# Performance work log

Hardware: AMD Instinct MI355X
Metric: run time of the kernel (lower is better)

Reference implementation:

```python
import jax, jax.numpy as jnp
import numpy as np

B_GR = 128    # graphs per batch
N0 = 512      # nodes per graph before pooling
E_PER = 4096  # edges per graph (kept static; pooled-away edges get weight 0)
H = 128       # hidden
F = 128       # num_features (== hidden)
C = 10        # num_classes
K_HOP = 3     # Jacobi polynomial order (hop_num)
A_J, B_J = 1.0, 1.0
EPS = 1e-5


def _bn(h, g, b):
    # training-mode BatchNorm1d: batch stats, biased variance
    m = jnp.mean(h, 0)
    v = jnp.mean((h - m) ** 2, 0)
    return (h - m) * jax.lax.rsqrt(v + EPS) * g + b


def _forward(x, convW, convb, bnW, bnB, bn7W, bn7B, attW, theta,
             lin1W, lin1b, lin2W, lin2b, lin3W, lin3b, src, dst):
    w = jnp.ones((src.shape[0],), x.dtype)  # edge weights; 0 => filtered edge
    n = N0
    h = x
    reads = []
    for i in range(5):
        N = B_GR * n
        # symmetric GCN normalization with self loops on the weighted graph
        deg = jax.ops.segment_sum(w, dst, num_segments=N) + 1.0
        dinv = jax.lax.rsqrt(deg)
        enorm = dinv[src] * dinv[dst] * w   # per-edge norm [E]
        snorm = dinv * dinv                 # self-loop norm [N]
        prop = lambda m_: jax.ops.segment_sum(enorm[:, None] * m_[src], dst, num_segments=N) + m_ * snorm[:, None]
        pvec = lambda v_: jax.ops.segment_sum(enorm * v_[src], dst, num_segments=N) + v_ * snorm
        # GCNConv -> BN -> ReLU
        h = prop(h @ convW[i]) + convb[i]
        h = jax.nn.relu(_bn(h, bnW[i], bnB[i]))
        # JacobiPool: Jacobi-polynomial diffusion of attention scores
        s0 = h @ attW[i]                    # [N]
        polys = [s0, 0.5 * ((A_J - B_J) * s0 + (A_J + B_J + 2.0) * pvec(s0))]
        for kk in range(2, K_HOP + 1):
            c0 = 2 * kk * (kk + A_J + B_J) * (2 * kk + A_J + B_J - 2)
            c1 = (2 * kk + A_J + B_J - 1) * (2 * kk + A_J + B_J) * (2 * kk + A_J + B_J - 2)
            c2 = (2 * kk + A_J + B_J - 1) * (A_J * A_J - B_J * B_J)
            c3 = 2 * (kk + A_J - 1) * (kk + B_J - 1) * (2 * kk + A_J + B_J)
            polys.append((c1 * pvec(polys[-1]) + c2 * polys[-1] - c3 * polys[-2]) / c0)
        score = sum(theta[i, j] * polys[j] for j in range(K_HOP + 1))
        # top-k node selection per graph (ratio 0.5 -> static k)
        k = n // 2
        _, idx = jax.lax.top_k(score.reshape(B_GR, n), k)
        sel = (idx + (jnp.arange(B_GR) * n)[:, None]).reshape(-1)  # global node ids [B*k]
        h = h[sel] * jnp.tanh(score[sel])[:, None]
        # remap/filter edges to surviving nodes (masked, static edge count)
        new_id = jnp.full((N,), -1, jnp.int32).at[sel].set(jnp.arange(B_GR * k, dtype=jnp.int32))
        ns, nd = new_id[src], new_id[dst]
        valid = (ns >= 0) & (nd >= 0) & (w > 0)
        w = valid.astype(x.dtype)
        src = jnp.where(valid, ns, 0)
        dst = jnp.where(valid, nd, 0)
        # readout: global max pool || global mean pool per graph
        xg = h.reshape(B_GR, k, H)
        reads.append(jnp.concatenate([xg.max(1), xg.mean(1)], -1))
        n = k
    g = sum(reads) / 5.0                    # [B, 2H]
    g = jax.nn.relu(_bn(g @ lin1W + lin1b, bnW[5], bnB[5]))
    g = jax.nn.relu(_bn(g @ lin2W + lin2b, bn7W, bn7B))
    return jax.nn.log_softmax(g @ lin3W + lin3b, -1)


def setup_inputs() -> dict:
    key = jax.random.key(0)
    ks = jax.random.split(key, 8)
    N = B_GR * N0
    E = B_GR * E_PER
    rng = np.random.default_rng(0)
    off = np.repeat(np.arange(B_GR, dtype=np.int32) * N0, E_PER)
    src = jnp.asarray(off + rng.integers(0, N0, E).astype(np.int32))
    dst = jnp.asarray(off + rng.integers(0, N0, E).astype(np.int32))
    s = 1.0 / np.sqrt(H)
    return {
        "x": jax.random.normal(ks[0], (N, F), jnp.float32),
        "convW": jax.random.normal(ks[1], (5, H, H), jnp.float32) * s,
        "convb": jnp.zeros((5, H), jnp.float32),
        "bnW": jnp.ones((6, H), jnp.float32),
        "bnB": jnp.zeros((6, H), jnp.float32),
        "bn7W": jnp.ones((H // 2,), jnp.float32),
        "bn7B": jnp.zeros((H // 2,), jnp.float32),
        "attW": jax.random.normal(ks[2], (5, H), jnp.float32) * s,
        "theta": jax.random.normal(ks[3], (5, K_HOP + 1), jnp.float32) * 0.5,
        "lin1W": jax.random.normal(ks[4], (2 * H, H), jnp.float32) * (1.0 / np.sqrt(2 * H)),
        "lin1b": jnp.zeros((H,), jnp.float32),
        "lin2W": jax.random.normal(ks[5], (H, H // 2), jnp.float32) * s,
        "lin2b": jnp.zeros((H // 2,), jnp.float32),
        "lin3W": jax.random.normal(ks[6], (H // 2, C), jnp.float32) * (1.0 / np.sqrt(H // 2)),
        "lin3b": jnp.zeros((C,), jnp.float32),
        "src": src,
        "dst": dst,
    }


def reference(x, convW, convb, bnW, bnB, bn7W, bn7B, attW, theta,
              lin1W, lin1b, lin2W, lin2b, lin3W, lin3b, src, dst):
    return _forward(x, convW, convb, bnW, bnB, bn7W, bn7B, attW, theta,
                    lin1W, lin1b, lin2W, lin2b, lin3W, lin3b, src, dst)
```

## Files before the change

kernel.cpp:

```cpp
#include <hip/hip_runtime.h>
#include <hip/hip_bf16.h>

#define B_GRAPH 128
#define ETOT    (128*4096)
#define N0G     (128*512)
#define HF      128

__global__ __launch_bounds__(256) void k_init(const int* __restrict__ s_in, const int* __restrict__ d_in_,
                                              int* __restrict__ srcw, int* __restrict__ dstw,
                                              float* __restrict__ wv, int2* __restrict__ csr,
                                              int2* __restrict__ rb2, float* __restrict__ dinvv,
                                              float* __restrict__ gacc, float* __restrict__ statsH,
                                              float* __restrict__ st0, float* __restrict__ st1,
                                              float* __restrict__ st2){
    int g = blockIdx.x, t = threadIdx.x;
    __shared__ int cnt[512];
    __shared__ int cur[512];
    __shared__ float dvl[512];
    for (int l = t; l < 512; l += 256) cnt[l] = 0;
    gacc[g*256 + t] = 0.f;
    if (g == 0){
        statsH[t] = 0.f; if (t < 128) statsH[256+t] = 0.f;
        st0[t] = 0.f; st1[t] = 0.f; st2[t] = 0.f;
    }
    __syncthreads();
    for (int j = t; j < 4096; j += 256){
        int e = g*4096 + j;
        int sg = s_in[e], dg = d_in_[e];
        srcw[e] = sg; dstw[e] = dg; wv[e] = 1.f;
        atomicAdd(&cnt[dg & 511], 1);
    }
    __syncthreads();
    int c0 = cnt[2*t], c1 = cnt[2*t+1];
    int pairsum = c0 + c1;
    cur[t] = pairsum;
    __syncthreads();
    for (int off = 1; off < 256; off <<= 1){
        int a = (t >= off) ? cur[t-off] : 0;
        __syncthreads();
        cur[t] += a;
        __syncthreads();
    }
    int begpair = cur[t] - pairsum;
    __syncthreads();
    cur[2*t]   = begpair;
    cur[2*t+1] = begpair + c0;
    __syncthreads();
    for (int l = t; l < 512; l += 256){
        rb2[g*512 + l] = make_int2(g*4096 + cur[l], cnt[l]);
        float dv = rsqrtf((float)cnt[l] + 1.f);
        dvl[l] = dv;
        dinvv[g*512 + l] = dv;
    }
    __syncthreads();
    for (int j = t; j < 4096; j += 256){
        int e = g*4096 + j;
        int sg = srcw[e], dl = dstw[e] & 511;
        int p = atomicAdd(&cur[dl], 1);
        csr[g*4096 + p] = make_int2(sg, __float_as_int(dvl[sg & 511]));
    }
}

__global__ __launch_bounds__(256) void k_gemm(const float* __restrict__ A, const float* __restrict__ Wg,
                                              float* __restrict__ C){
    __shared__ float Ws[64*HF];
    int tx = threadIdx.x & 15, ty = threadIdx.x >> 4;
    int r0 = blockIdx.x*64 + ty*4, c0 = tx*4;
    float acc[4][8];
    #pragma unroll
    for (int j=0;j<4;++j)
        #pragma unroll
        for (int l=0;l<8;++l) acc[j][l] = 0.f;
    for (int kh = 0; kh < 2; ++kh){
        __syncthreads();
        {
            float4* d4 = (float4*)Ws;
            const float4* s4 = (const float4*)(Wg + kh*64*HF);
            for (int i = threadIdx.x; i < 64*HF/4; i += 256) d4[i] = s4[i];
        }
        __syncthreads();
        for (int k4 = 0; k4 < 16; ++k4){
            float4 av[4];
            #pragma unroll
            for (int j=0;j<4;++j)
                av[j] = *(const float4*)(A + (size_t)(r0+j)*HF + kh*64 + k4*4);
            #pragma unroll
            for (int kk=0; kk<4; ++kk){
                int kl = k4*4 + kk;
                float4 w0 = *(const float4*)(Ws + kl*HF + c0);
                float4 w1 = *(const float4*)(Ws + kl*HF + c0 + 64);
                #pragma unroll
                for (int j=0;j<4;++j){
                    float a = reinterpret_cast<const float*>(&av[j])[kk];
                    acc[j][0] += a*w0.x; acc[j][1] += a*w0.y; acc[j][2] += a*w0.z; acc[j][3] += a*w0.w;
                    acc[j][4] += a*w1.x; acc[j][5] += a*w1.y; acc[j][6] += a*w1.z; acc[j][7] += a*w1.w;
                }
            }
        }
    }
    #pragma unroll
    for (int j=0;j<4;++j){
        *(float4*)(C + (size_t)(r0+j)*HF + c0)      = make_float4(acc[j][0],acc[j][1],acc[j][2],acc[j][3]);
        *(float4*)(C + (size_t)(r0+j)*HF + c0 + 64) = make_float4(acc[j][4],acc[j][5],acc[j][6],acc[j][7]);
    }
}

__global__ __launch_bounds__(256) void k_prop(const float* __restrict__ Y, const float* __restrict__ cb,
                                              const int2* __restrict__ rb2, const int2* __restrict__ cp,
                                              const float* __restrict__ dinv,
                                              float* __restrict__ X, int n, int lb, int Nn){
    int xcd = blockIdx.x & 7, c = blockIdx.x >> 3;
    int g = xcd*16 + (c >> lb);
    int m = c & ((1 << lb) - 1);
    int v = g*n + m*8 + (threadIdx.x >> 5);
    int f4 = threadIdx.x & 31;
    float dv = dinv[v];
    float4 y = *(const float4*)(Y + (size_t)v*HF + f4*4);
    float4 acc = make_float4(0.f, 0.f, 0.f, 0.f);
    int2 rb = rb2[v];
    int e0 = rb.x, e1 = rb.x + rb.y;
    for (int j = e0; j < e1; ++j){
        int2 e = cp[j];
        int s = e.x & (Nn - 1);
        float en = __int_as_float(e.y);
        float4 h = *(const float4*)(Y + (size_t)s*HF + f4*4);
        acc.x += en*h.x; acc.y += en*h.y; acc.z += en*h.z; acc.w += en*h.w;
    }
    int f = f4*4;
    acc.x = y.x*dv*dv + dv*acc.x + cb[f];
    acc.y = y.y*dv*dv + dv*acc.y + cb[f+1];
    acc.z = y.z*dv*dv + dv*acc.z + cb[f+2];
    acc.w = y.w*dv*dv + dv*acc.w + cb[f+3];
    *(float4*)(X + (size_t)v*HF + f) = acc;
}

__global__ __launch_bounds__(256) void k_bnstats(const float* __restrict__ X, float* __restrict__ stats){
    int c = threadIdx.x & 127, h = threadIdx.x >> 7;
    int r0 = blockIdx.x * 256;
    float s = 0.f, s2 = 0.f;
    for (int r = r0 + h; r < r0 + 256; r += 2){
        float x = X[(size_t)r*HF + c];
        s += x; s2 += x*x;
    }
    __shared__ float l1[256], l2[256];
    l1[threadIdx.x] = s; l2[threadIdx.x] = s2;
    __syncthreads();
    if (threadIdx.x < 128){
        atomicAdd(&stats[c],     l1[threadIdx.x] + l1[threadIdx.x+128]);
        atomicAdd(&stats[128+c], l2[threadIdx.x] + l2[threadIdx.x+128]);
    }
}

union KSmem {
    struct {
        int2  eds[4096]; int2 rbl[512];
        float dvv[512], p0[512], p1[512], p2[512];
        float ss[512]; int si[512]; float tss[256]; int nid[512];
        int   cntN[256], curN[256]; float dvn[256];
        float bna[128], bnb[128]; float red[1024];
    } gr;
    struct { float Ws[64*HF]; float red[32*HF]; } cv;
};

__global__ __launch_bounds__(1024) void k_graph(
    const float* __restrict__ H, const float* __restrict__ stats,
    const float* __restrict__ gw, const float* __restrict__ gb,
    const float* __restrict__ aw, const float* __restrict__ th,
    const int2* __restrict__ rb2, int2* __restrict__ csr, const float* __restrict__ dinv,
    int* __restrict__ srcw, int* __restrict__ dstw, float* __restrict__ wv,
    float* __restrict__ P, float* __restrict__ gacc,
    int2* __restrict__ rb2n, float* __restrict__ dinvn,
    float* __restrict__ stZero, float* __restrict__ stAcc,
    const float* __restrict__ Wnext, const float* __restrict__ cbNext,
    float* __restrict__ Gnext, float* __restrict__ Hnext,
    float invN, float ca2, float cc2, float ca3, float cc3,
    int n, int last)
{
    int g = blockIdx.x, t = threadIdx.x;
    int k = n >> 1;
    __shared__ KSmem sm;

    if (t < 256) stZero[t] = 0.f;
    if (t < 128){
        float mean = stats[t]*invN;
        float var  = stats[128+t]*invN - mean*mean;
        float iv   = rsqrtf(var + 1e-5f);
        sm.gr.bna[t] = iv*gw[t];
        sm.gr.bnb[t] = gb[t] - mean*iv*gw[t];
    }
    for (int l = t; l < n; l += 1024){
        int2 rb = rb2[g*n + l];
        sm.gr.rbl[l] = make_int2(rb.x - g*4096, rb.y);
        sm.gr.dvv[l] = dinv[g*n + l];
    }
    __syncthreads();
    int medg = sm.gr.rbl[n-1].x + sm.gr.rbl[n-1].y;
    for (int j = t; j < medg; j += 1024){
        int2 e = csr[g*4096 + j];
        sm.gr.eds[j] = make_int2(e.x & (n-1), e.y);
    }
    int lane = t & 63, wid = t >> 6;
    for (int l = wid; l < n; l += 16){
        const float* hp = H + ((size_t)g*n + l)*HF;
        float a0 = hp[lane], a1 = hp[lane+64];
        float v0 = fmaxf(a0*sm.gr.bna[lane]    + sm.gr.bnb[lane],    0.f) * aw[lane];
        float v1 = fmaxf(a1*sm.gr.bna[lane+64] + sm.gr.bnb[lane+64], 0.f) * aw[lane+64];
        float p = v0 + v1;
        for (int off = 32; off; off >>= 1) p += __shfl_down(p, off);
        if (lane == 0) sm.gr.p0[l] = p;
    }
    __syncthreads();
    for (int l = t; l < n; l += 1024){
        int2 rc = sm.gr.rbl[l];
        float acc = 0.f;
        for (int j = 0; j < rc.y; ++j){
            int2 e = sm.gr.eds[rc.x + j];
            acc += __int_as_float(e.y) * sm.gr.p0[e.x];
        }
        float dv = sm.gr.dvv[l];
        sm.gr.p1[l] = 2.f*(sm.gr.p0[l]*dv*dv + dv*acc);
    }
    __syncthreads();
    for (int l = t; l < n; l += 1024){
        int2 rc = sm.gr.rbl[l];
        float acc = 0.f;
        for (int j = 0; j < rc.y; ++j){
            int2 e = sm.gr.eds[rc.x + j];
            acc += __int_as_float(e.y) * sm.gr.p1[e.x];
        }
        float dv = sm.gr.dvv[l];
        sm.gr.p2[l] = ca2*(sm.gr.p1[l]*dv*dv + dv*acc) + cc2*sm.gr.p0[l];
    }
    __syncthreads();
    float t0v = th[0], t1v = th[1], t2c = th[2], t3v = th[3];
    for (int l = t; l < n; l += 1024){
        int2 rc = sm.gr.rbl[l];
        float acc = 0.f;
        for (int j = 0; j < rc.y; ++j){
            int2 e = sm.gr.eds[rc.x + j];
            acc += __int_as_float(e.y) * sm.gr.p2[e.x];
        }
        float dv = sm.gr.dvv[l];
        float tv = sm.gr.p2[l]*dv*dv + dv*acc;
        float p3 = ca3*tv + cc3*sm.gr.p1[l];
        sm.gr.ss[l] = t0v*sm.gr.p0[l] + t1v*sm.gr.p1[l] + t2c*sm.gr.p2[l] + t3v*p3;
        sm.gr.si[l] = l;
    }
    __syncthreads();
    for (int size = 2; size <= n; size <<= 1){
        for (int stride = size >> 1; stride > 0; stride >>= 1){
            for (int i = t; i < n; i += 1024){
                int j = i ^ stride;
                if (j > i){
                    bool asc = ((i & size) == 0);
                    float s1 = sm.gr.ss[i], s2 = sm.gr.ss[j];
                    int   i1 = sm.gr.si[i], i2 = sm.gr.si[j];
                    bool gt = (s1 < s2) || (s1 == s2 && i1 > i2);
                    if (gt == asc){ sm.gr.ss[i] = s2; sm.gr.ss[j] = s1; sm.gr.si[i] = i2; sm.gr.si[j] = i1; }
                }
            }
            __syncthreads();
        }
    }
    for (int l = t; l < n; l += 1024) sm.gr.nid[l] = -1;
    __syncthreads();
    for (int r = t; r < k; r += 1024){
        sm.gr.nid[sm.gr.si[r]] = r;
        sm.gr.tss[r] = tanhf(sm.gr.ss[r]);
    }
    __syncthreads();
    {
        int f = t & 127, rl = t >> 7;
        float af = sm.gr.bna[f], bf = sm.gr.bnb[f];
        float mx = -3.4e38f, smv = 0.f;
        for (int r = rl; r < k; r += 8){
            int old = sm.gr.si[r];
            float hv = H[((size_t)g*n + old)*HF + f];
            float v = fmaxf(hv*af + bf, 0.f) * sm.gr.tss[r];
            P[((size_t)g*k + r)*HF + f] = v;
            mx = fmaxf(mx, v); smv += v;
        }
        sm.gr.red[t] = mx;
        __syncthreads();
        if (t < 512) sm.gr.red[t] = fmaxf(sm.gr.red[t], sm.gr.red[t+512]);
        __syncthreads();
        if (t < 256) sm.gr.red[t] = fmaxf(sm.gr.red[t], sm.gr.red[t+256]);
        __syncthreads();
        if (t < 128) gacc[g*256 + t] += fmaxf(sm.gr.red[t], sm.gr.red[t+128]);
        __syncthreads();
        sm.gr.red[t] = smv;
        __syncthreads();
        if (t < 512) sm.gr.red[t] += sm.gr.red[t+512];
        __syncthreads();
        if (t < 256) sm.gr.red[t] += sm.gr.red[t+256];
        __syncthreads();
        if (t < 128) gacc[g*256 + 128 + t] += (sm.gr.red[t] + sm.gr.red[t+128]) / (float)k;
    }
    if (last) return;
    __syncthreads();
    if (t < k) sm.gr.cntN[t] = 0;
    __syncthreads();
    for (int j = t; j < 4096; j += 1024){
        int e = g*4096 + j;
        float we = wv[e];
        int valid = 0, ns = 0, nd = 0;
        if (we > 0.5f){
            int sl = srcw[e] & (n-1);
            int dl = dstw[e] & (n-1);
            ns = sm.gr.nid[sl]; nd = sm.gr.nid[dl];
            valid = (ns >= 0) && (nd >= 0);
        }
        if (valid){
            srcw[e] = g*k + ns; dstw[e] = g*k + nd; wv[e] = 1.f;
            atomicAdd(&sm.gr.cntN[nd], 1);
        } else {
            srcw[e] = 0; dstw[e] = 0; wv[e] = 0.f;
        }
    }
    __syncthreads();
    int c = (t < 256) ? ((t < k) ? sm.gr.cntN[t] : 0) : 0;
    if (t < 256) sm.gr.si[t] = c;
    __syncthreads();
    for (int off = 1; off < 256; off <<= 1){
        int a = 0;
        if (t < 256 && t >= off) a = sm.gr.si[t-off];
        __syncthreads();
        if (t < 256) sm.gr.si[t] += a;
        __syncthreads();
    }
    if (t < k){
        int beg = sm.gr.si[t] - c;
        rb2n[g*k + t] = make_int2(g*4096 + beg, c);
        float dv = rsqrtf((float)c + 1.f);
        dinvn[g*k + t] = dv;
        sm.gr.dvn[t] = dv;
        sm.gr.curN[t] = beg;
    }
    __syncthreads();
    for (int j = t; j < 4096; j += 1024){
        int e = g*4096 + j;
        if (wv[e] > 0.5f){
            int sg = srcw[e], dl = dstw[e] & (k-1);
            int p = atomicAdd(&sm.gr.curN[dl], 1);
            csr[g*4096 + p] = make_int2(sg, __float_as_int(sm.gr.dvn[sg & (k-1)]));
        }
    }
    __syncthreads();
    int Nn2 = B_GRAPH * k;
    {
        int sub = t >> 8, t8 = t & 255, tx = t8 & 15, ty = t8 >> 4;
        int cc0 = tx*4;
        int nT = (k + 255) >> 8;
        for (int tile = 0; tile < nT; ++tile){
            int r0 = tile*256 + sub*64 + ty*4;
            bool act = (r0 < k);
            float acc[4][8];
            #pragma unroll
            for (int j=0;j<4;++j)
                #pragma unroll
                for (int l=0;l<8;++l) acc[j][l] = 0.f;
            for (int kh = 0; kh < 2; ++kh){
                __syncthreads();
                {
                    float4* d4 = (float4*)sm.cv.Ws;
                    const float4* s4 = (const float4*)(Wnext + kh*64*HF);
                    #pragma unroll
                    for (int i2 = 0; i2 < 2; ++i2) d4[t + i2*1024] = s4[t + i2*1024];
                }
                __syncthreads();
                if (act){
                    for (int k4 = 0; k4 < 16; ++k4){
                        float4 av[4];
                        #pragma unroll
                        for (int j=0;j<4;++j)
                            av[j] = *(const float4*)(P + ((size_t)g*k + r0 + j)*HF + kh*64 + k4*4);
                        #pragma unroll
                        for (int kk=0; kk<4; ++kk){
                            int kl = k4*4 + kk;
                            float4 w0 = *(const float4*)(sm.cv.Ws + kl*HF + cc0);
                            float4 w1 = *(const float4*)(sm.cv.Ws + kl*HF + cc0 + 64);
                            #pragma unroll
                            for (int j=0;j<4;++j){
                                float aa = reinterpret_cast<const float*>(&av[j])[kk];
                                acc[j][0] += aa*w0.x; acc[j][1] += aa*w0.y; acc[j][2] += aa*w0.z; acc[j][3] += aa*w0.w;
                                acc[j][4] += aa*w1.x; acc[j][5] += aa*w1.y; acc[j][6] += aa*w1.z; acc[j][7] += aa*w1.w;
                            }
                        }
                    }
                }
            }
            if (act){
                #pragma unroll
                for (int j=0;j<4;++j){
                    *(float4*)(Gnext + ((size_t)g*k + r0 + j)*HF + cc0)      = make_float4(acc[j][0],acc[j][1],acc[j][2],acc[j][3]);
                    *(float4*)(Gnext + ((size_t)g*k + r0 + j)*HF + cc0 + 64) = make_float4(acc[j][4],acc[j][5],acc[j][6],acc[j][7]);
                }
            }
        }
    }
    __syncthreads();
    {
        int f = (t & 31)*4;
        float4 s  = make_float4(0.f,0.f,0.f,0.f);
        float4 s2 = make_float4(0.f,0.f,0.f,0.f);
        float cb0 = cbNext[f], cb1 = cbNext[f+1], cb2 = cbNext[f+2], cb3 = cbNext[f+3];
        for (int l = t >> 5; l < k; l += 32){
            int v = g*k + l;
            float dv = dinvn[v];
            float4 y = *(const float4*)(Gnext + (size_t)v*HF + f);
            float4 acc = make_float4(0.f,0.f,0.f,0.f);
            int2 rb = rb2n[v];
            int e1 = rb.x + rb.y;
            for (int j = rb.x; j < e1; ++j){
                int2 e = csr[j];
                int sN = e.x & (Nn2 - 1);
                float en = __int_as_float(e.y);
                float4 h = *(const float4*)(Gnext + (size_t)sN*HF + f);
                acc.x += en*h.x; acc.y += en*h.y; acc.z += en*h.z; acc.w += en*h.w;
            }
            acc.x = y.x*dv*dv + dv*acc.x + cb0;
            acc.y = y.y*dv*dv + dv*acc.y + cb1;
            acc.z = y.z*dv*dv + dv*acc.z + cb2;
            acc.w = y.w*dv*dv + dv*acc.w + cb3;
            *(float4*)(Hnext + (size_t)v*HF + f) = acc;
            s.x += acc.x; s.y += acc.y; s.z += acc.z; s.w += acc.w;
            s2.x += acc.x*acc.x; s2.y += acc.y*acc.y; s2.z += acc.z*acc.z; s2.w += acc.w*acc.w;
        }
        int base = (t >> 5)*HF + f;
        __syncthreads();
        *(float4*)&sm.cv.red[base] = s;
        __syncthreads();
        if (t < 128){
            float a = 0.f;
            #pragma unroll
            for (int j = 0; j < 32; ++j) a += sm.cv.red[j*HF + t];
            atomicAdd(&stAcc[t], a);
        }
        __syncthreads();
        *(float4*)&sm.cv.red[base] = s2;
        __syncthreads();
        if (t < 128){
            float a = 0.f;
            #pragma unroll
            for (int j = 0; j < 32; ++j) a += sm.cv.red[j*HF + t];
            atomicAdd(&stAcc[128+t], a);
        }
    }
}

__global__ __launch_bounds__(256) void k_head1(const float* __restrict__ gacc, const float* __restrict__ W1,
                                               const float* __restrict__ b1, float* __restrict__ t1,
                                               float* __restrict__ sh){
    int r = blockIdx.x;
    int c = threadIdx.x & 127, h = threadIdx.x >> 7;
    __shared__ float gs[256];
    __shared__ float red[256];
    gs[threadIdx.x] = gacc[r*256 + threadIdx.x];
    __syncthreads();
    float s = 0.f;
    #pragma unroll
    for (int kk = 0; kk < 128; ++kk)
        s += gs[h*128 + kk] * W1[(h*128 + kk)*128 + c];
    red[threadIdx.x] = s;
    __syncthreads();
    if (h == 0){
        float v = (red[c] + red[c+128]) * 0.2f + b1[c];
        t1[r*128 + c] = v;
        atomicAdd(&sh[c], v);
        atomicAdd(&sh[128 + c], v*v);
    }
}
__global__ __launch_bounds__(128) void k_head2(const float* __restrict__ t1, const float* __restrict__ gw,
                                               const float* __restrict__ gb, const float* __restrict__ W2,
                                               const float* __restrict__ b2, float* __restrict__ sh,
                                               float* __restrict__ t2){
    int r = blockIdx.x, t = threadIdx.x;
    int cc = t & 63, h = t >> 6;
    __shared__ float row[128];
    __shared__ float red[128];
    {
        float mean = sh[t] * (1.f/128.f);
        float var  = sh[128+t]*(1.f/128.f) - mean*mean;
        float iv   = rsqrtf(var + 1e-5f);
        float v = (t1[r*128+t] - mean)*iv*gw[t] + gb[t];
        row[t] = fmaxf(v, 0.f);
    }
    __syncthreads();
    float s = 0.f;
    #pragma unroll
    for (int kk = 0; kk < 64; ++kk)
        s += row[h*64+kk] * W2[(h*64+kk)*64 + cc];
    red[t] = s;
    __syncthreads();
    if (h == 0){
        float v = red[cc] + red[cc+64] + b2[cc];
        t2[r*64+cc] = v;
        atomicAdd(&sh[256+cc], v);
        atomicAdd(&sh[320+cc], v*v);
    }
}
__global__ __launch_bounds__(64) void k_head3(const float* __restrict__ t2, const float* __restrict__ gw,
                                              const float* __restrict__ gb, const float* __restrict__ W3,
                                              const float* __restrict__ b3, const float* __restrict__ sh,
                                              float* __restrict__ out){
    int r = blockIdx.x, t = threadIdx.x;
    float mean = sh[256+t]*(1.f/128.f);
    float var  = sh[320+t]*(1.f/128.f) - mean*mean;
    float iv   = rsqrtf(var + 1e-5f);
    float v = fmaxf((t2[r*64+t]-mean)*iv*gw[t] + gb[t], 0.f);
    float lg[10];
    #pragma unroll
    for (int j = 0; j < 10; ++j){
        float p = v * W3[t*10 + j];
        for (int off = 32; off; off >>= 1) p += __shfl_down(p, off);
        lg[j] = p;
    }
    if (t == 0){
        float m = -3.4e38f;
        #pragma unroll
        for (int j = 0; j < 10; ++j){ lg[j] += b3[j]; m = fmaxf(m, lg[j]); }
        float se = 0.f;
        #pragma unroll
        for (int j = 0; j < 10; ++j) se += expf(lg[j] - m);
        float l = logf(se) + m;
        #pragma unroll
        for (int j = 0; j < 10; ++j) out[r*10 + j] = lg[j] - l;
    }
}

extern "C" void kernel_launch(void* const* d_in, const int* in_sizes, int n_in,
                              void* d_out, int out_size, void* d_ws, size_t ws_size,
                              hipStream_t stream){
    const float* x     = (const float*)d_in[0];
    const float* convW = (const float*)d_in[1];
    const float* convb = (const float*)d_in[2];
    const float* bnW   = (const float*)d_in[3];
    const float* bnB   = (const float*)d_in[4];
    const float* bn7W  = (const float*)d_in[5];
    const float* bn7B  = (const float*)d_in[6];
    const float* attW  = (const float*)d_in[7];
    const float* theta = (const float*)d_in[8];
    const float* lin1W = (const float*)d_in[9];
    const float* lin1b = (const float*)d_in[10];
    const float* lin2W = (const float*)d_in[11];
    const float* lin2b = (const float*)d_in[12];
    const float* lin3W = (const float*)d_in[13];
    const float* lin3b = (const float*)d_in[14];
    const int*   src0  = (const int*)d_in[15];
    const int*   dst0  = (const int*)d_in[16];

    char* base = (char*)d_ws;
    size_t off = 0;
    auto take = [&](size_t bytes) -> void* {
        void* p = base + off;
        off = (off + bytes + 255) & ~(size_t)255;
        return p;
    };
    float* bufGP = (float*)take((size_t)N0G*HF*4);
    float* bufHA = (float*)take((size_t)N0G*HF*4);
    float* bufHB = (float*)take((size_t)(N0G/2)*HF*4);
    int*   srcw  = (int*)  take((size_t)ETOT*4);
    int*   dstw  = (int*)  take((size_t)ETOT*4);
    float* w     = (float*)take((size_t)ETOT*4);
    int2*  csr_p = (int2*) take((size_t)ETOT*8);
    int2*  rb2A  = (int2*) take((size_t)N0G*8);
    int2*  rb2B  = (int2*) take((size_t)N0G*8);
    float* dinvA = (float*)take((size_t)N0G*4);
    float* dinvB = (float*)take((size_t)N0G*4);
    float* st[3];
    st[0] = (float*)take(256*4);
    st[1] = (float*)take(256*4);
    st[2] = (float*)take(256*4);
    float* gacc  = (float*)take((size_t)B_GRAPH*256*4);
    float* t1    = (float*)take((size_t)B_GRAPH*128*4);
    float* t2    = (float*)take((size_t)B_GRAPH*64*4);
    float* statsH= (float*)take(384*4);

    auto coef = [](int kk, float& ca, float& cc){
        double a = 1.0, b = 1.0;
        double c0 = 2.0*kk*(kk+a+b)*(2.0*kk+a+b-2.0);
        double c1 = (2.0*kk+a+b-1.0)*(2.0*kk+a+b)*(2.0*kk+a+b-2.0);
        double c3 = 2.0*(kk+a-1.0)*(kk+b-1.0)*(2.0*kk+a+b);
        ca = (float)(c1/c0); cc = (float)(-c3/c0);
    };
    float ca2, cc2, ca3, cc3;
    coef(2, ca2, cc2);
    coef(3, ca3, cc3);

    k_init<<<B_GRAPH, 256, 0, stream>>>(src0, dst0, srcw, dstw, w, csr_p, rb2A, dinvA,
                                        gacc, statsH, st[0], st[1], st[2]);

    float* G = bufGP + (size_t)4*1024*1024;
    k_gemm<<<N0G/64, 256, 0, stream>>>(x, convW, bufGP);
    k_prop<<<N0G/8, 256, 0, stream>>>(bufGP, convb, rb2A, csr_p, dinvA, bufHA, 512, 6, N0G);
    k_bnstats<<<N0G/256, 256, 0, stream>>>(bufHA, st[0]);

    for (int i = 0; i < 5; ++i){
        int n = 512 >> i;
        int Nn = B_GRAPH*n;
        int2*  rb_cur = (i & 1) ? rb2B : rb2A;
        int2*  rb_nxt = (i & 1) ? rb2A : rb2B;
        float* dv_cur = (i & 1) ? dinvB : dinvA;
        float* dv_nxt = (i & 1) ? dinvA : dinvB;
        float* Hcur = (i & 1) ? bufHB : bufHA;
        float* Hnxt = (i & 1) ? bufHA : bufHB;
        int wnext = (i < 4) ? (i + 1) : 4;

        k_graph<<<B_GRAPH, 1024, 0, stream>>>(Hcur, st[i % 3], bnW + i*HF, bnB + i*HF, attW + i*HF,
                                              theta + i*4, rb_cur, csr_p, dv_cur,
                                              srcw, dstw, w, bufGP, gacc, rb_nxt, dv_nxt,
                                              st[(i + 2) % 3], st[(i + 1) % 3],
                                              convW + (size_t)wnext*HF*HF, convb + wnext*HF,
                                              G, Hnxt,
                                              1.0f/(float)Nn, ca2, cc2, ca3, cc3, n, (i == 4) ? 1 : 0);
    }

    k_head1<<<B_GRAPH, 256, 0, stream>>>(gacc, lin1W, lin1b, t1, statsH);
    k_head2<<<B_GRAPH, 128, 0, stream>>>(t1, bnW + 5*HF, bnB + 5*HF, lin2W, lin2b, statsH, t2);
    k_head3<<<B_GRAPH, 64, 0, stream>>>(t2, bn7W, bn7B, lin3W, lin3b, statsH, (float*)d_out);
}
```

Measured before the change: 476.2 us.

## Fuse init with GEMM, BN stats into prop, head1 into last graph kernel

Merges the CSR-building init kernel and the first GEMM into one launch with block-index dispatch, folds the BatchNorm column statistics into the propagation kernel via shared-memory reduction, and moves the lin1 head into the final graph-kernel pass. BN stat accumulators are split into 8 per-XCD slices to reduce atomic contention, with readers summing the slices. This removes three launches and a full re-read of the layer-0 activations, at the cost of larger stat buffers, extra shared memory in prop, and atomics on more addresses.

```diff
diff --git a/kernel.cpp b/kernel.cpp
--- a/kernel.cpp
+++ b/kernel.cpp
@@ -5,114 +5,121 @@
 #define ETOT    (128*4096)
 #define N0G     (128*512)
 #define HF      128
-
-__global__ __launch_bounds__(256) void k_init(const int* __restrict__ s_in, const int* __restrict__ d_in_,
-                                              int* __restrict__ srcw, int* __restrict__ dstw,
-                                              float* __restrict__ wv, int2* __restrict__ csr,
-                                              int2* __restrict__ rb2, float* __restrict__ dinvv,
-                                              float* __restrict__ gacc, float* __restrict__ statsH,
-                                              float* __restrict__ st0, float* __restrict__ st1,
-                                              float* __restrict__ st2){
-    int g = blockIdx.x, t = threadIdx.x;
-    __shared__ int cnt[512];
-    __shared__ int cur[512];
-    __shared__ float dvl[512];
-    for (int l = t; l < 512; l += 256) cnt[l] = 0;
-    gacc[g*256 + t] = 0.f;
-    if (g == 0){
-        statsH[t] = 0.f; if (t < 128) statsH[256+t] = 0.f;
-        st0[t] = 0.f; st1[t] = 0.f; st2[t] = 0.f;
-    }
-    __syncthreads();
-    for (int j = t; j < 4096; j += 256){
-        int e = g*4096 + j;
-        int sg = s_in[e], dg = d_in_[e];
-        srcw[e] = sg; dstw[e] = dg; wv[e] = 1.f;
-        atomicAdd(&cnt[dg & 511], 1);
-    }
-    __syncthreads();
-    int c0 = cnt[2*t], c1 = cnt[2*t+1];
-    int pairsum = c0 + c1;
-    cur[t] = pairsum;
-    __syncthreads();
-    for (int off = 1; off < 256; off <<= 1){
-        int a = (t >= off) ? cur[t-off] : 0;
-        __syncthreads();
-        cur[t] += a;
-        __syncthreads();
-    }
-    int begpair = cur[t] - pairsum;
-    __syncthreads();
-    cur[2*t]   = begpair;
-    cur[2*t+1] = begpair + c0;
-    __syncthreads();
-    for (int l = t; l < 512; l += 256){
-        rb2[g*512 + l] = make_int2(g*4096 + cur[l], cnt[l]);
-        float dv = rsqrtf((float)cnt[l] + 1.f);
-        dvl[l] = dv;
-        dinvv[g*512 + l] = dv;
-    }
-    __syncthreads();
-    for (int j = t; j < 4096; j += 256){
-        int e = g*4096 + j;
-        int sg = srcw[e], dl = dstw[e] & 511;
-        int p = atomicAdd(&cur[dl], 1);
-        csr[g*4096 + p] = make_int2(sg, __float_as_int(dvl[sg & 511]));
-    }
-}
-
-__global__ __launch_bounds__(256) void k_gemm(const float* __restrict__ A, const float* __restrict__ Wg,
-                                              float* __restrict__ C){
-    __shared__ float Ws[64*HF];
-    int tx = threadIdx.x & 15, ty = threadIdx.x >> 4;
-    int r0 = blockIdx.x*64 + ty*4, c0 = tx*4;
-    float acc[4][8];
-    #pragma unroll
-    for (int j=0;j<4;++j)
-        #pragma unroll
-        for (int l=0;l<8;++l) acc[j][l] = 0.f;
-    for (int kh = 0; kh < 2; ++kh){
-        __syncthreads();
-        {
-            float4* d4 = (float4*)Ws;
-            const float4* s4 = (const float4*)(Wg + kh*64*HF);
-            for (int i = threadIdx.x; i < 64*HF/4; i += 256) d4[i] = s4[i];
-        }
-        __syncthreads();
-        for (int k4 = 0; k4 < 16; ++k4){
-            float4 av[4];
+#define STSZ    2048
+
+union IGSmem {
+    float Ws[64*HF];
+    struct { int cnt[512]; int cur[512]; float dvl[512]; } ini;
+};
+
+__global__ __launch_bounds__(256) void k_init_gemm(
+    const float* __restrict__ A, const float* __restrict__ Wg, float* __restrict__ C,
+    const int* __restrict__ s_in, const int* __restrict__ d_in_,
+    int* __restrict__ srcw, int* __restrict__ dstw, float* __restrict__ wv,
+    int2* __restrict__ csr, int2* __restrict__ rb2, float* __restrict__ dinvv,
+    float* __restrict__ gacc, float* __restrict__ statsH,
+    float* __restrict__ st0, float* __restrict__ st1, float* __restrict__ st2)
+{
+    __shared__ IGSmem sm;
+    int t = threadIdx.x;
+    if (blockIdx.x < 1024){
+        int tx = t & 15, ty = t >> 4;
+        int r0 = blockIdx.x*64 + ty*4, c0 = tx*4;
+        float acc[4][8];
+        #pragma unroll
+        for (int j=0;j<4;++j)
             #pragma unroll
-            for (int j=0;j<4;++j)
-                av[j] = *(const float4*)(A + (size_t)(r0+j)*HF + kh*64 + k4*4);
-            #pragma unroll
-            for (int kk=0; kk<4; ++kk){
-                int kl = k4*4 + kk;
-                float4 w0 = *(const float4*)(Ws + kl*HF + c0);
-                float4 w1 = *(const float4*)(Ws + kl*HF + c0 + 64);
+            for (int l=0;l<8;++l) acc[j][l] = 0.f;
+        for (int kh = 0; kh < 2; ++kh){
+            __syncthreads();
+            {
+                float4* d4 = (float4*)sm.Ws;
+                const float4* s4 = (const float4*)(Wg + kh*64*HF);
+                for (int i = t; i < 64*HF/4; i += 256) d4[i] = s4[i];
+            }
+            __syncthreads();
+            for (int k4 = 0; k4 < 16; ++k4){
+                float4 av[4];
                 #pragma unroll
-                for (int j=0;j<4;++j){
-                    float a = reinterpret_cast<const float*>(&av[j])[kk];
-                    acc[j][0] += a*w0.x; acc[j][1] += a*w0.y; acc[j][2] += a*w0.z; acc[j][3] += a*w0.w;
-                    acc[j][4] += a*w1.x; acc[j][5] += a*w1.y; acc[j][6] += a*w1.z; acc[j][7] += a*w1.w;
+                for (int j=0;j<4;++j)
+                    av[j] = *(const float4*)(A + (size_t)(r0+j)*HF + kh*64 + k4*4);
+                #pragma unroll
+                for (int kk=0; kk<4; ++kk){
+                    int kl = k4*4 + kk;
+                    float4 w0 = *(const float4*)(sm.Ws + kl*HF + c0);
+                    float4 w1 = *(const float4*)(sm.Ws + kl*HF + c0 + 64);
+                    #pragma unroll
+                    for (int j=0;j<4;++j){
+                        float a = reinterpret_cast<const float*>(&av[j])[kk];
+                        acc[j][0] += a*w0.x; acc[j][1] += a*w0.y; acc[j][2] += a*w0.z; acc[j][3] += a*w0.w;
+                        acc[j][4] += a*w1.x; acc[j][5] += a*w1.y; acc[j][6] += a*w1.z; acc[j][7] += a*w1.w;
+                    }
                 }
             }
         }
-    }
-    #pragma unroll
-    for (int j=0;j<4;++j){
-        *(float4*)(C + (size_t)(r0+j)*HF + c0)      = make_float4(acc[j][0],acc[j][1],acc[j][2],acc[j][3]);
-        *(float4*)(C + (size_t)(r0+j)*HF + c0 + 64) = make_float4(acc[j][4],acc[j][5],acc[j][6],acc[j][7]);
+        #pragma unroll
+        for (int j=0;j<4;++j){
+            *(float4*)(C + (size_t)(r0+j)*HF + c0)      = make_float4(acc[j][0],acc[j][1],acc[j][2],acc[j][3]);
+            *(float4*)(C + (size_t)(r0+j)*HF + c0 + 64) = make_float4(acc[j][4],acc[j][5],acc[j][6],acc[j][7]);
+        }
+    } else {
+        int g = blockIdx.x - 1024;
+        for (int l = t; l < 512; l += 256) sm.ini.cnt[l] = 0;
+        gacc[g*256 + t] = 0.f;
+        if (g == 0){
+            if (t < 256){ statsH[t] = 0.f; if (t < 128) statsH[256+t] = 0.f; }
+            for (int i = t; i < STSZ; i += 256){ st0[i] = 0.f; st1[i] = 0.f; st2[i] = 0.f; }
+        }
+        __syncthreads();
+        for (int j = t; j < 4096; j += 256){
+            int e = g*4096 + j;
+            int sg = s_in[e], dg = d_in_[e];
+            srcw[e] = sg; dstw[e] = dg; wv[e] = 1.f;
+            atomicAdd(&sm.ini.cnt[dg & 511], 1);
+        }
+        __syncthreads();
+        int c0 = sm.ini.cnt[2*t], c1 = sm.ini.cnt[2*t+1];
+        int pairsum = c0 + c1;
+        sm.ini.cur[t] = pairsum;
+        __syncthreads();
+        for (int off = 1; off < 256; off <<= 1){
+            int a = (t >= off) ? sm.ini.cur[t-off] : 0;
+            __syncthreads();
+            sm.ini.cur[t] += a;
+            __syncthreads();
+        }
+        int begpair = sm.ini.cur[t] - pairsum;
+        __syncthreads();
+        sm.ini.cur[2*t]   = begpair;
+        sm.ini.cur[2*t+1] = begpair + c0;
+        __syncthreads();
+        for (int l = t; l < 512; l += 256){
+            rb2[g*512 + l] = make_int2(g*4096 + sm.ini.cur[l], sm.ini.cnt[l]);
+            float dv = rsqrtf((float)sm.ini.cnt[l] + 1.f);
+            sm.ini.dvl[l] = dv;
+            dinvv[g*512 + l] = dv;
+        }
+        __syncthreads();
+        for (int j = t; j < 4096; j += 256){
+            int e = g*4096 + j;
+            int sg = srcw[e], dl = dstw[e] & 511;
+            int p = atomicAdd(&sm.ini.cur[dl], 1);
+            csr[g*4096 + p] = make_int2(sg, __float_as_int(sm.ini.dvl[sg & 511]));
+        }
     }
 }
 
-__global__ __launch_bounds__(256) void k_prop(const float* __restrict__ Y, const float* __restrict__ cb,
-                                              const int2* __restrict__ rb2, const int2* __restrict__ cp,
-                                              const float* __restrict__ dinv,
-                                              float* __restrict__ X, int n, int lb, int Nn){
+__global__ __launch_bounds__(256) void k_prop_stats(const float* __restrict__ Y, const float* __restrict__ cb,
+                                                    const int2* __restrict__ rb2, const int2* __restrict__ cp,
+                                                    const float* __restrict__ dinv,
+                                                    float* __restrict__ X, float* __restrict__ st,
+                                                    int n, int lb, int Nn){
+    __shared__ float rs[1024], rq[1024];
     int xcd = blockIdx.x & 7, c = blockIdx.x >> 3;
     int g = xcd*16 + (c >> lb);
     int m = c & ((1 << lb) - 1);
-    int v = g*n + m*8 + (threadIdx.x >> 5);
+    int nd = threadIdx.x >> 5;
+    int v = g*n + m*8 + nd;
     int f4 = threadIdx.x & 31;
     float dv = dinv[v];
     float4 y = *(const float4*)(Y + (size_t)v*HF + f4*4);
@@ -132,22 +139,16 @@
     acc.z = y.z*dv*dv + dv*acc.z + cb[f+2];
     acc.w = y.w*dv*dv + dv*acc.w + cb[f+3];
     *(float4*)(X + (size_t)v*HF + f) = acc;
-}
-
-__global__ __launch_bounds__(256) void k_bnstats(const float* __restrict__ X, float* __restrict__ stats){
-    int c = threadIdx.x & 127, h = threadIdx.x >> 7;
-    int r0 = blockIdx.x * 256;
-    float s = 0.f, s2 = 0.f;
-    for (int r = r0 + h; r < r0 + 256; r += 2){
-        float x = X[(size_t)r*HF + c];
-        s += x; s2 += x*x;
-    }
-    __shared__ float l1[256], l2[256];
-    l1[threadIdx.x] = s; l2[threadIdx.x] = s2;
+    *(float4*)&rs[nd*HF + f] = acc;
+    *(float4*)&rq[nd*HF + f] = make_float4(acc.x*acc.x, acc.y*acc.y, acc.z*acc.z, acc.w*acc.w);
     __syncthreads();
     if (threadIdx.x < 128){
-        atomicAdd(&stats[c],     l1[threadIdx.x] + l1[threadIdx.x+128]);
-        atomicAdd(&stats[128+c], l2[threadIdx.x] + l2[threadIdx.x+128]);
+        int tt = threadIdx.x;
+        float s = 0.f, q = 0.f;
+        #pragma unroll
+        for (int j = 0; j < 8; ++j){ s += rs[j*HF + tt]; q += rq[j*HF + tt]; }
+        atomicAdd(&st[xcd*256 + tt], s);
+        atomicAdd(&st[xcd*256 + 128 + tt], q);
     }
 }
 
@@ -173,6 +174,8 @@
     float* __restrict__ stZero, float* __restrict__ stAcc,
     const float* __restrict__ Wnext, const float* __restrict__ cbNext,
     float* __restrict__ Gnext, float* __restrict__ Hnext,
+    const float* __restrict__ lin1W, const float* __restrict__ lin1b,
+    float* __restrict__ t1g, float* __restrict__ statsH,
     float invN, float ca2, float cc2, float ca3, float cc3,
     int n, int last)
 {
@@ -180,10 +183,13 @@
     int k = n >> 1;
     __shared__ KSmem sm;
 
-    if (t < 256) stZero[t] = 0.f;
+    for (int i = t; i < STSZ; i += 1024) stZero[i] = 0.f;
     if (t < 128){
-        float mean = stats[t]*invN;
-        float var  = stats[128+t]*invN - mean*mean;
+        float s = 0.f, q = 0.f;
+        #pragma unroll
+        for (int b2 = 0; b2 < 8; ++b2){ s += stats[b2*256 + t]; q += stats[b2*256 + 128 + t]; }
+        float mean = s*invN;
+        float var  = q*invN - mean*mean;
         float iv   = rsqrtf(var + 1e-5f);
         sm.gr.bna[t] = iv*gw[t];
         sm.gr.bnb[t] = gb[t] - mean*iv*gw[t];
@@ -296,7 +302,28 @@
         __syncthreads();
         if (t < 128) gacc[g*256 + 128 + t] += (sm.gr.red[t] + sm.gr.red[t+128]) / (float)k;
     }
-    if (last) return;
+    if (last){
+        __syncthreads();
+        int c = t & 127, h = t >> 7;
+        float s = 0.f;
+        int k0 = h*32;
+        #pragma unroll
+        for (int kk = 0; kk < 32; ++kk)
+            s += gacc[g*256 + k0 + kk] * lin1W[(k0 + kk)*128 + c];
+        sm.gr.red[t] = s;
+        __syncthreads();
+        if (t < 512) sm.gr.red[t] += sm.gr.red[t+512];
+        __syncthreads();
+        if (t < 256) sm.gr.red[t] += sm.gr.red[t+256];
+        __syncthreads();
+        if (t < 128){
+            float v = (sm.gr.red[t] + sm.gr.red[t+128]) * 0.2f + lin1b[t];
+            t1g[g*128 + t] = v;
+            atomicAdd(&statsH[t], v);
+            atomicAdd(&statsH[128+t], v*v);
+        }
+        return;
+    }
     __syncthreads();
     if (t < k) sm.gr.cntN[t] = 0;
     __syncthreads();
@@ -434,7 +461,7 @@
             float a = 0.f;
             #pragma unroll
             for (int j = 0; j < 32; ++j) a += sm.cv.red[j*HF + t];
-            atomicAdd(&stAcc[t], a);
+            atomicAdd(&stAcc[(g & 7)*256 + t], a);
         }
         __syncthreads();
         *(float4*)&sm.cv.red[base] = s2;
@@ -443,33 +470,11 @@
             float a = 0.f;
             #pragma unroll
             for (int j = 0; j < 32; ++j) a += sm.cv.red[j*HF + t];
-            atomicAdd(&stAcc[128+t], a);
+            atomicAdd(&stAcc[(g & 7)*256 + 128 + t], a);
         }
     }
 }
 
-__global__ __launch_bounds__(256) void k_head1(const float* __restrict__ gacc, const float* __restrict__ W1,
-                                               const float* __restrict__ b1, float* __restrict__ t1,
-                                               float* __restrict__ sh){
-    int r = blockIdx.x;
-    int c = threadIdx.x & 127, h = threadIdx.x >> 7;
-    __shared__ float gs[256];
-    __shared__ float red[256];
-    gs[threadIdx.x] = gacc[r*256 + threadIdx.x];
-    __syncthreads();
-    float s = 0.f;
-    #pragma unroll
-    for (int kk = 0; kk < 128; ++kk)
-        s += gs[h*128 + kk] * W1[(h*128 + kk)*128 + c];
-    red[threadIdx.x] = s;
-    __syncthreads();
-    if (h == 0){
-        float v = (red[c] + red[c+128]) * 0.2f + b1[c];
-        t1[r*128 + c] = v;
-        atomicAdd(&sh[c], v);
-        atomicAdd(&sh[128 + c], v*v);
-    }
-}
 __global__ __launch_bounds__(128) void k_head2(const float* __restrict__ t1, const float* __restrict__ gw,
                                                const float* __restrict__ gb, const float* __restrict__ W2,
                                                const float* __restrict__ b2, float* __restrict__ sh,
@@ -568,9 +573,9 @@
     float* dinvA = (float*)take((size_t)N0G*4);
     float* dinvB = (float*)take((size_t)N0G*4);
     float* st[3];
-    st[0] = (float*)take(256*4);
-    st[1] = (float*)take(256*4);
-    st[2] = (float*)take(256*4);
+    st[0] = (float*)take(STSZ*4);
+    st[1] = (float*)take(STSZ*4);
+    st[2] = (float*)take(STSZ*4);
     float* gacc  = (float*)take((size_t)B_GRAPH*256*4);
     float* t1    = (float*)take((size_t)B_GRAPH*128*4);
     float* t2    = (float*)take((size_t)B_GRAPH*64*4);
@@ -587,13 +592,12 @@
     coef(2, ca2, cc2);
     coef(3, ca3, cc3);
 
-    k_init<<<B_GRAPH, 256, 0, stream>>>(src0, dst0, srcw, dstw, w, csr_p, rb2A, dinvA,
-                                        gacc, statsH, st[0], st[1], st[2]);
+    k_init_gemm<<<1024 + B_GRAPH, 256, 0, stream>>>(x, convW, bufGP,
+                                                    src0, dst0, srcw, dstw, w, csr_p, rb2A, dinvA,
+                                                    gacc, statsH, st[0], st[1], st[2]);
+    k_prop_stats<<<N0G/8, 256, 0, stream>>>(bufGP, convb, rb2A, csr_p, dinvA, bufHA, st[0], 512, 6, N0G);
 
     float* G = bufGP + (size_t)4*1024*1024;
-    k_gemm<<<N0G/64, 256, 0, stream>>>(x, convW, bufGP);
-    k_prop<<<N0G/8, 256, 0, stream>>>(bufGP, convb, rb2A, csr_p, dinvA, bufHA, 512, 6, N0G);
-    k_bnstats<<<N0G/256, 256, 0, stream>>>(bufHA, st[0]);
 
     for (int i = 0; i < 5; ++i){
         int n = 512 >> i;
@@ -612,10 +616,10 @@
                                               st[(i + 2) % 3], st[(i + 1) % 3],
                                               convW + (size_t)wnext*HF*HF, convb + wnext*HF,
                                               G, Hnxt,
+                                              lin1W, lin1b, t1, statsH,
                                               1.0f/(float)Nn, ca2, cc2, ca3, cc3, n, (i == 4) ? 1 : 0);
     }
 
-    k_head1<<<B_GRAPH, 256, 0, stream>>>(gacc, lin1W, lin1b, t1, statsH);
     k_head2<<<B_GRAPH, 128, 0, stream>>>(t1, bnW + 5*HF, bnB + 5*HF, lin2W, lin2b, statsH, t2);
     k_head3<<<B_GRAPH, 64, 0, stream>>>(t2, bn7W, bn7B, lin3W, lin3b, statsH, (float*)d_out);
 }
```

Measured after the change: 444.0 us. 1.07x faster.
